# Optimization experiments

Measured on AMD Instinct MI355X. Metric: run time of the kernel, lower is better.

## Reference

```python
import jax, jax.numpy as jnp
import numpy as np

TAU = 2.0      # LIF membrane time constant (spikingjelly default-style, decay_input=True)
VTH = 0.5      # v_threshold from init
S = 4          # time_steps
EPS = 1e-5     # BatchNorm eps
ALPHA = 4.0    # surrogate sigmoid alpha (spikingjelly Sigmoid default)

@jax.custom_vjp
def spike(x):
    # Heaviside forward (spikingjelly: x >= 0 -> 1)
    return (x >= 0.0).astype(x.dtype)

def _spike_fwd(x):
    return spike(x), x

def _spike_bwd(x, g):
    sg = jax.nn.sigmoid(ALPHA * x)
    return (g * ALPHA * sg * (1.0 - sg),)

spike.defvjp(_spike_fwd, _spike_bwd)

def bn(y, gamma, beta, mean, var):
    # inference-mode BatchNorm2d over channel axis 1; y: (B, C, T, V)
    inv = gamma * jax.lax.rsqrt(var + EPS)
    return y * inv[None, :, None, None] + (beta - mean * inv)[None, :, None, None]


def setup_inputs() -> dict:
    key = jax.random.key(0)
    ks = jax.random.split(key, 16)
    B, T, C, V, H, NC = 16, 512, 3, 16, 128, 12
    inp = {
        "x": jax.random.normal(ks[0], (B, T, C, V), dtype=jnp.float32),
        "w1": jax.random.normal(ks[1], (H, C), dtype=jnp.float32) * (1.0 / np.sqrt(C)),
        "b1": jax.random.normal(ks[2], (H,), dtype=jnp.float32) * 0.01,
        "g1": jnp.ones((H,), jnp.float32),
        "be1": jnp.zeros((H,), jnp.float32),
        "m1": jax.random.normal(ks[3], (H,), dtype=jnp.float32) * 0.1,
        "rv1": jax.random.uniform(ks[4], (H,), dtype=jnp.float32) + 0.5,
        "w2": jax.random.normal(ks[5], (H, H), dtype=jnp.float32) * (1.0 / np.sqrt(H)),
        "b2": jax.random.normal(ks[6], (H,), dtype=jnp.float32) * 0.01,
        "g2": jnp.ones((H,), jnp.float32),
        "be2": jnp.zeros((H,), jnp.float32),
        "m2": jax.random.normal(ks[7], (H,), dtype=jnp.float32) * 0.1,
        "rv2": jax.random.uniform(ks[8], (H,), dtype=jnp.float32) + 0.5,
        "wc": jax.random.normal(ks[9], (NC, H), dtype=jnp.float32) * (1.0 / np.sqrt(H)),
        "bc": jax.random.normal(ks[10], (NC,), dtype=jnp.float32) * 0.01,
    }
    return inp


def reference(x, w1, b1, g1, be1, m1, rv1, w2, b2, g2, be2, m2, rv2, wc, bc):
    # x: (B, T, C, V) -> channels-first (B, C, T, V) as in torch permute
    xc = jnp.transpose(x, (0, 2, 1, 3))
    # fc1 1x1 conv + BN; input identical across all S steps, so compute once
    h1 = bn(jnp.einsum('bctv,oc->botv', xc, w1) + b1[None, :, None, None],
            g1, be1, m1, rv1)  # (B, H, T, V)

    def step(carry, _):
        v1s, v2s, acc = carry
        # LIF1: decay_input=True, v_reset=0 hard reset
        v1n = v1s + (h1 - v1s) / TAU
        s1 = spike(v1n - VTH)
        v1n = v1n * (1.0 - s1)
        # fc2 1x1 conv + BN on spikes
        h2 = bn(jnp.einsum('botv,po->bptv', s1, w2) + b2[None, :, None, None],
                g2, be2, m2, rv2)
        # LIF2
        v2n = v2s + (h2 - v2s) / TAU
        s2 = spike(v2n - VTH)
        v2n = v2n * (1.0 - s2)
        return (v1n, v2n, acc + s2), None

    z = jnp.zeros_like(h1)
    (_, _, acc), _ = jax.lax.scan(step, (z, z, z), None, length=S)
    # mean over S, then mean over T and V -> (B, H); dropout is identity in eval
    feat = (acc / S).mean(axis=(2, 3))
    return feat @ wc.T + bc
```

## Files before the change

### kernel.cpp

```cpp
#include <hip/hip_runtime.h>
#include <hip/hip_bf16.h>
#include <stdint.h>
#include <math.h>

#define B_ 16
#define T_ 512
#define V_ 16
#define H_ 128
#define NC_ 12

typedef float v2f __attribute__((ext_vector_type(2)));
typedef __attribute__((ext_vector_type(8))) short s8frag;
typedef __attribute__((ext_vector_type(4))) float f4frag;
typedef unsigned long long u64;


__global__ __launch_bounds__(1024) void zero_feat_kernel(float* __restrict__ feat) {
    int i = blockIdx.x * 1024 + threadIdx.x;
    if (i < B_ * H_) feat[i] = 0.f;
}

__global__ __launch_bounds__(1024, 4) void snn_main(
    const float* __restrict__ x,
    const float* __restrict__ w1, const float* __restrict__ b1,
    const float* __restrict__ g1, const float* __restrict__ be1,
    const float* __restrict__ m1, const float* __restrict__ rv1,
    const float* __restrict__ w2, const float* __restrict__ b2,
    const float* __restrict__ g2, const float* __restrict__ be2,
    const float* __restrict__ m2, const float* __restrict__ rv2,
    float* __restrict__ feat)
{
    __shared__ union {
        unsigned short Bw[2 * H_ * H_];
        uint4 afrag[16 * 4 * 64];
    } u;
    __shared__ u64 mask_lds[64 * 8];
    __shared__ u64 lut[16];
    __shared__ float red[8 * 16];

    const int tid  = threadIdx.x;
    const int lane = tid & 63;
    const int wave = tid >> 6;
    const int b     = blockIdx.x >> 6;
    const int chunk = blockIdx.x & 63;
    const int slice = wave & 7;
    const int kg    = lane >> 4;

    if (tid < 16) {
        u64 v = 0;
        #pragma unroll
        for (int j = 0; j < 4; ++j)
            if ((tid >> j) & 1) v |= (u64)0x3F80u << (16 * j);
        lut[tid] = v;
    }

    for (int i = tid; i < H_ * H_; i += 1024) {
        float w = w2[i];
        __hip_bfloat16 hb = __float2bfloat16(w);
        float hf = __bfloat162float(hb);
        __hip_bfloat16 lb = __float2bfloat16(w - hf);
        u.Bw[i]            = *(unsigned short*)&hb;
        u.Bw[H_ * H_ + i]  = *(unsigned short*)&lb;
    }

    const int p = lane, q = lane + 64;
    v2f w0v = { w1[p*3+0], w1[q*3+0] };
    v2f w1v = { w1[p*3+1], w1[q*3+1] };
    v2f w2v = { w1[p*3+2], w1[q*3+2] };
    v2f b1v = { b1[p], b1[q] };
    float i1a = g1[p] * (float)(1.0 / sqrt((double)(rv1[p] + 1e-5f)));
    float i1b = g1[q] * (float)(1.0 / sqrt((double)(rv1[q] + 1e-5f)));
    v2f i1v = { i1a, i1b };
    v2f d1v = { be1[p] - m1[p] * i1a, be1[q] - m1[q] * i1b };
    const int ch = slice * 16 + (lane & 15);
    float i2c = g2[ch] * (float)(1.0 / sqrt((double)(rv2[ch] + 1e-5f)));
    float d2c = be2[ch] - m2[ch] * i2c;
    float b2c = b2[ch];

    __syncthreads();

    s8frag bhi[4], blo[4];
    #pragma unroll
    for (int c = 0; c < 4; ++c) {
        int idx = ch * H_ + c * 32 + kg * 8;
        bhi[c] = *(const s8frag*)&u.Bw[idx];
        blo[c] = *(const s8frag*)&u.Bw[H_ * H_ + idx];
    }
    __syncthreads();

    float facc = 0.f;
    const int tile_own = wave;
    const int tbase = (wave >> 3) * 8;

    for (int g = 0; g < 2; ++g) {
        #pragma unroll
        for (int i = 0; i < 4; ++i) {
            int sl   = wave + 16 * i;
            int site = chunk * 128 + g * 64 + sl;
            int t = site >> 4, v = site & 15;
            const float* xp = x + ((size_t)(b * T_ + t) * 3) * V_ + v;
            float x0 = xp[0], x1 = xp[V_], x2 = xp[2 * V_];

            v2f h1 = ((x0 * w0v + x1 * w1v + x2 * w2v) + b1v) * i1v + d1v;
            v2f v1t = h1 * 0.5f;
            v2f v2t = v1t + h1 * 0.25f;
            v2f v3t = v2t + (h1 - v2t) * 0.5f;
            v2f v4t = v3t + (h1 - v3t) * 0.5f;

            u64 t1a = __ballot(v1t.x >= 0.5f), t2a = __ballot(v2t.x >= 0.5f);
            u64 t3a = __ballot(v3t.x >= 0.5f), t4a = __ballot(v4t.x >= 0.5f);
            u64 t1b = __ballot(v1t.y >= 0.5f), t2b = __ballot(v2t.y >= 0.5f);
            u64 t3b = __ballot(v3t.y >= 0.5f), t4b = __ballot(v4t.y >= 0.5f);
            u64 s3a = t1a | (t3a & ~t2a), s3b = t1b | (t3b & ~t2b);
            u64 s4a = t2a | (t4a & ~t3a), s4b = t2b | (t4b & ~t3b);

            if (lane < 8) {
                int stp = lane >> 1; bool hf = lane & 1;
                u64 vm;
                if      (stp == 0) vm = hf ? t1b : t1a;
                else if (stp == 1) vm = hf ? t2b : t2a;
                else if (stp == 2) vm = hf ? s3b : s3a;
                else               vm = hf ? s4b : s4a;
                mask_lds[sl * 8 + lane] = vm;
            }
        }
        __syncthreads();

        {
            int r   = lane & 15;
            int sl  = tile_own * 4 + (r >> 2);
            int stp = r & 3;
            const unsigned char* mb = (const unsigned char*)&mask_lds[sl * 8 + stp * 2];
            #pragma unroll
            for (int c = 0; c < 4; ++c) {
                unsigned int bt = mb[c * 4 + kg];
                u64 lo = lut[bt & 15], hi = lut[bt >> 4];
                uint4 fr;
                fr.x = (unsigned)lo; fr.y = (unsigned)(lo >> 32);
                fr.z = (unsigned)hi; fr.w = (unsigned)(hi >> 32);
                u.afrag[(tile_own * 4 + c) * 64 + lane] = fr;
            }
        }
        __syncthreads();

        for (int j = 0; j < 8; ++j) {
            int tl = tbase + j;
            s8frag a0 = *(const s8frag*)&u.afrag[(tl * 4 + 0) * 64 + lane];
            s8frag a1 = *(const s8frag*)&u.afrag[(tl * 4 + 1) * 64 + lane];
            s8frag a2 = *(const s8frag*)&u.afrag[(tl * 4 + 2) * 64 + lane];
            s8frag a3 = *(const s8frag*)&u.afrag[(tl * 4 + 3) * 64 + lane];
            f4frag acc = { 0.f, 0.f, 0.f, 0.f };
            acc = __builtin_amdgcn_mfma_f32_16x16x32_bf16(a0, bhi[0], acc, 0, 0, 0);
            acc = __builtin_amdgcn_mfma_f32_16x16x32_bf16(a1, bhi[1], acc, 0, 0, 0);
            acc = __builtin_amdgcn_mfma_f32_16x16x32_bf16(a2, bhi[2], acc, 0, 0, 0);
            acc = __builtin_amdgcn_mfma_f32_16x16x32_bf16(a3, bhi[3], acc, 0, 0, 0);
            acc = __builtin_amdgcn_mfma_f32_16x16x32_bf16(a0, blo[0], acc, 0, 0, 0);
            acc = __builtin_amdgcn_mfma_f32_16x16x32_bf16(a1, blo[1], acc, 0, 0, 0);
            acc = __builtin_amdgcn_mfma_f32_16x16x32_bf16(a2, blo[2], acc, 0, 0, 0);
            acc = __builtin_amdgcn_mfma_f32_16x16x32_bf16(a3, blo[3], acc, 0, 0, 0);

            float vv = 0.f;
            #pragma unroll
            for (int s = 0; s < 4; ++s) {
                float h2 = (acc[s] + b2c) * i2c + d2c;
                vv = vv + (h2 - vv) * 0.5f;
                bool sp = vv >= 0.5f;
                vv = sp ? 0.f : vv;
                facc += sp ? 1.f : 0.f;
            }
        }
        __syncthreads();
    }

    facc += __shfl_down(facc, 32);
    facc += __shfl_down(facc, 16);
    if (wave < 8) {
        if (lane < 16) red[slice * 16 + lane] = facc;
    }
    __syncthreads();
    if (wave >= 8 && lane < 16) {
        atomicAdd(&feat[b * H_ + ch], red[slice * 16 + lane] + facc);
    }
}

__global__ __launch_bounds__(128) void classifier_kernel(
    const float* __restrict__ feat,
    const float* __restrict__ wc,
    const float* __restrict__ bc,
    float* __restrict__ out) {
    __shared__ float fb[H_];
    int b = blockIdx.x, t = threadIdx.x;
    fb[t] = feat[b * H_ + t] * (1.0f / 32768.0f);
    __syncthreads();
    if (t < NC_) {
        float s = 0.f;
        for (int h = 0; h < H_; ++h) s += fb[h] * wc[t * H_ + h];
        out[b * NC_ + t] = s + bc[t];
    }
}

extern "C" void kernel_launch(void* const* d_in, const int* in_sizes, int n_in,
                              void* d_out, int out_size, void* d_ws, size_t ws_size,
                              hipStream_t stream) {
    const float* x   = (const float*)d_in[0];
    const float* w1  = (const float*)d_in[1];
    const float* b1  = (const float*)d_in[2];
    const float* g1  = (const float*)d_in[3];
    const float* be1 = (const float*)d_in[4];
    const float* m1  = (const float*)d_in[5];
    const float* rv1 = (const float*)d_in[6];
    const float* w2  = (const float*)d_in[7];
    const float* b2  = (const float*)d_in[8];
    const float* g2  = (const float*)d_in[9];
    const float* be2 = (const float*)d_in[10];
    const float* m2  = (const float*)d_in[11];
    const float* rv2 = (const float*)d_in[12];
    const float* wc  = (const float*)d_in[13];
    const float* bc  = (const float*)d_in[14];
    float* feat = (float*)d_ws;
    float* out  = (float*)d_out;

    zero_feat_kernel<<<2, 1024, 0, stream>>>(feat);
    snn_main<<<1024, 1024, 0, stream>>>(x, w1, b1, g1, be1, m1, rv1,
                                        w2, b2, g2, be2, m2, rv2, feat);
    classifier_kernel<<<B_, 128, 0, stream>>>(feat, wc, bc, out);
}
```

Measured before the change: 154.9 us.

## Precompute bf16 split weights once and pipeline spike-mask build with MFMA

Moves the hi/lo bf16 split of w2 into a prep kernel run once per call, so each block loads B fragments straight from global memory instead of rebuilding them in LDS. Blocks shrink to 256 threads, and each wave now owns 32 output channels across all sites. Spike masks are double-buffered in LDS, so the MFMA work for the previous round overlaps fragment construction for the next, with one barrier per round. A bit-arithmetic expand replaces the LUT. The trade is more blocks and more atomics, plus higher register pressure from holding two channel sets of B fragments.

```diff
diff --git a/kernel.cpp b/kernel.cpp
--- a/kernel.cpp
+++ b/kernel.cpp
@@ -14,54 +14,56 @@
 typedef __attribute__((ext_vector_type(4))) float f4frag;
 typedef unsigned long long u64;
 
-
-__global__ __launch_bounds__(1024) void zero_feat_kernel(float* __restrict__ feat) {
-    int i = blockIdx.x * 1024 + threadIdx.x;
+#define WS_W2L_OFF  32768
+#define WS_FEAT_OFF 65536
+
+__global__ __launch_bounds__(256) void prep_kernel(const float* __restrict__ w2,
+                                                   unsigned short* __restrict__ w2h,
+                                                   unsigned short* __restrict__ w2l,
+                                                   float* __restrict__ feat) {
+    int i = blockIdx.x * 256 + threadIdx.x;
+    if (i < H_ * H_) {
+        float w = w2[i];
+        __hip_bfloat16 hb = __float2bfloat16(w);
+        float hf = __bfloat162float(hb);
+        __hip_bfloat16 lb = __float2bfloat16(w - hf);
+        w2h[i] = *(unsigned short*)&hb;
+        w2l[i] = *(unsigned short*)&lb;
+    }
     if (i < B_ * H_) feat[i] = 0.f;
 }
 
-__global__ __launch_bounds__(1024, 4) void snn_main(
+__device__ __forceinline__ uint4 expand8(unsigned bt) {
+    uint4 r;
+    r.x = ((bt      & 1u) * 0x3F80u) | (((bt >> 1) & 1u) * 0x3F800000u);
+    r.y = (((bt >> 2) & 1u) * 0x3F80u) | (((bt >> 3) & 1u) * 0x3F800000u);
+    r.z = (((bt >> 4) & 1u) * 0x3F80u) | (((bt >> 5) & 1u) * 0x3F800000u);
+    r.w = (((bt >> 6) & 1u) * 0x3F80u) | (((bt >> 7) & 1u) * 0x3F800000u);
+    return r;
+}
+
+#define ROUNDS 4
+__global__ __launch_bounds__(256, 3) void snn_main(
     const float* __restrict__ x,
     const float* __restrict__ w1, const float* __restrict__ b1,
     const float* __restrict__ g1, const float* __restrict__ be1,
     const float* __restrict__ m1, const float* __restrict__ rv1,
-    const float* __restrict__ w2, const float* __restrict__ b2,
+    const unsigned short* __restrict__ w2h, const unsigned short* __restrict__ w2l,
+    const float* __restrict__ b2,
     const float* __restrict__ g2, const float* __restrict__ be2,
     const float* __restrict__ m2, const float* __restrict__ rv2,
     float* __restrict__ feat)
 {
-    __shared__ union {
-        unsigned short Bw[2 * H_ * H_];
-        uint4 afrag[16 * 4 * 64];
-    } u;
-    __shared__ u64 mask_lds[64 * 8];
-    __shared__ u64 lut[16];
-    __shared__ float red[8 * 16];
+    __shared__ uint4 afrag[2][4][4][64];
+    __shared__ uint4 msk[4][16];
 
     const int tid  = threadIdx.x;
     const int lane = tid & 63;
-    const int wave = tid >> 6;
-    const int b     = blockIdx.x >> 6;
-    const int chunk = blockIdx.x & 63;
-    const int slice = wave & 7;
-    const int kg    = lane >> 4;
-
-    if (tid < 16) {
-        u64 v = 0;
-        #pragma unroll
-        for (int j = 0; j < 4; ++j)
-            if ((tid >> j) & 1) v |= (u64)0x3F80u << (16 * j);
-        lut[tid] = v;
-    }
-
-    for (int i = tid; i < H_ * H_; i += 1024) {
-        float w = w2[i];
-        __hip_bfloat16 hb = __float2bfloat16(w);
-        float hf = __bfloat162float(hb);
-        __hip_bfloat16 lb = __float2bfloat16(w - hf);
-        u.Bw[i]            = *(unsigned short*)&hb;
-        u.Bw[H_ * H_ + i]  = *(unsigned short*)&lb;
-    }
+    const int wv   = tid >> 6;
+    const int kg   = lane >> 4;
+    const int nl   = lane & 15;
+    const int bb   = blockIdx.x >> 7;
+    const int sbase = (blockIdx.x & 127) * (ROUNDS * 16);
 
     const int p = lane, q = lane + 64;
     v2f w0v = { w1[p*3+0], w1[q*3+0] };
@@ -72,33 +74,71 @@
     float i1b = g1[q] * (float)(1.0 / sqrt((double)(rv1[q] + 1e-5f)));
     v2f i1v = { i1a, i1b };
     v2f d1v = { be1[p] - m1[p] * i1a, be1[q] - m1[q] * i1b };
-    const int ch = slice * 16 + (lane & 15);
-    float i2c = g2[ch] * (float)(1.0 / sqrt((double)(rv2[ch] + 1e-5f)));
-    float d2c = be2[ch] - m2[ch] * i2c;
-    float b2c = b2[ch];
-
-    __syncthreads();
-
-    s8frag bhi[4], blo[4];
+
+    const int ch0 = wv * 32 + nl;
+    const int ch1 = ch0 + 16;
+    float i2c0 = g2[ch0] * (float)(1.0 / sqrt((double)(rv2[ch0] + 1e-5f)));
+    float d2c0 = be2[ch0] - m2[ch0] * i2c0;
+    float b2c0 = b2[ch0];
+    float i2c1 = g2[ch1] * (float)(1.0 / sqrt((double)(rv2[ch1] + 1e-5f)));
+    float d2c1 = be2[ch1] - m2[ch1] * i2c1;
+    float b2c1 = b2[ch1];
+
+    s8frag bh0[4], bl0[4], bh1[4], bl1[4];
     #pragma unroll
     for (int c = 0; c < 4; ++c) {
-        int idx = ch * H_ + c * 32 + kg * 8;
-        bhi[c] = *(const s8frag*)&u.Bw[idx];
-        blo[c] = *(const s8frag*)&u.Bw[H_ * H_ + idx];
-    }
-    __syncthreads();
-
-    float facc = 0.f;
-    const int tile_own = wave;
-    const int tbase = (wave >> 3) * 8;
-
-    for (int g = 0; g < 2; ++g) {
+        int i0 = ch0 * H_ + c * 32 + kg * 8;
+        int i1 = ch1 * H_ + c * 32 + kg * 8;
+        bh0[c] = *(const s8frag*)&w2h[i0];
+        bl0[c] = *(const s8frag*)&w2l[i0];
+        bh1[c] = *(const s8frag*)&w2h[i1];
+        bl1[c] = *(const s8frag*)&w2l[i1];
+    }
+
+    float facc0 = 0.f, facc1 = 0.f;
+
+    #define CONSUME(BUF)                                                        \
+        for (int tt = 0; tt < 4; ++tt) {                                        \
+            s8frag a0 = *(const s8frag*)&afrag[BUF][tt][0][lane];               \
+            s8frag a1 = *(const s8frag*)&afrag[BUF][tt][1][lane];               \
+            s8frag a2 = *(const s8frag*)&afrag[BUF][tt][2][lane];               \
+            s8frag a3 = *(const s8frag*)&afrag[BUF][tt][3][lane];               \
+            f4frag acc0 = {0.f,0.f,0.f,0.f}, acc1 = {0.f,0.f,0.f,0.f};          \
+            acc0 = __builtin_amdgcn_mfma_f32_16x16x32_bf16(a0, bh0[0], acc0, 0,0,0); \
+            acc0 = __builtin_amdgcn_mfma_f32_16x16x32_bf16(a1, bh0[1], acc0, 0,0,0); \
+            acc0 = __builtin_amdgcn_mfma_f32_16x16x32_bf16(a2, bh0[2], acc0, 0,0,0); \
+            acc0 = __builtin_amdgcn_mfma_f32_16x16x32_bf16(a3, bh0[3], acc0, 0,0,0); \
+            acc0 = __builtin_amdgcn_mfma_f32_16x16x32_bf16(a0, bl0[0], acc0, 0,0,0); \
+            acc0 = __builtin_amdgcn_mfma_f32_16x16x32_bf16(a1, bl0[1], acc0, 0,0,0); \
+            acc0 = __builtin_amdgcn_mfma_f32_16x16x32_bf16(a2, bl0[2], acc0, 0,0,0); \
+            acc0 = __builtin_amdgcn_mfma_f32_16x16x32_bf16(a3, bl0[3], acc0, 0,0,0); \
+            acc1 = __builtin_amdgcn_mfma_f32_16x16x32_bf16(a0, bh1[0], acc1, 0,0,0); \
+            acc1 = __builtin_amdgcn_mfma_f32_16x16x32_bf16(a1, bh1[1], acc1, 0,0,0); \
+            acc1 = __builtin_amdgcn_mfma_f32_16x16x32_bf16(a2, bh1[2], acc1, 0,0,0); \
+            acc1 = __builtin_amdgcn_mfma_f32_16x16x32_bf16(a3, bh1[3], acc1, 0,0,0); \
+            acc1 = __builtin_amdgcn_mfma_f32_16x16x32_bf16(a0, bl1[0], acc1, 0,0,0); \
+            acc1 = __builtin_amdgcn_mfma_f32_16x16x32_bf16(a1, bl1[1], acc1, 0,0,0); \
+            acc1 = __builtin_amdgcn_mfma_f32_16x16x32_bf16(a2, bl1[2], acc1, 0,0,0); \
+            acc1 = __builtin_amdgcn_mfma_f32_16x16x32_bf16(a3, bl1[3], acc1, 0,0,0); \
+            float v0 = 0.f, v1 = 0.f;                                           \
+            _Pragma("unroll")                                                   \
+            for (int s = 0; s < 4; ++s) {                                       \
+                float h20 = (acc0[s] + b2c0) * i2c0 + d2c0;                     \
+                float h21 = (acc1[s] + b2c1) * i2c1 + d2c1;                     \
+                v0 = v0 + (h20 - v0) * 0.5f;                                    \
+                v1 = v1 + (h21 - v1) * 0.5f;                                    \
+                bool s0 = v0 >= 0.5f, s1 = v1 >= 0.5f;                          \
+                v0 = s0 ? 0.f : v0;  v1 = s1 ? 0.f : v1;                        \
+                facc0 += s0 ? 1.f : 0.f;  facc1 += s1 ? 1.f : 0.f;              \
+            }                                                                   \
+        }
+
+    for (int r = 0; r < ROUNDS; ++r) {
         #pragma unroll
         for (int i = 0; i < 4; ++i) {
-            int sl   = wave + 16 * i;
-            int site = chunk * 128 + g * 64 + sl;
+            int site = sbase + r * 16 + wv * 4 + i;
             int t = site >> 4, v = site & 15;
-            const float* xp = x + ((size_t)(b * T_ + t) * 3) * V_ + v;
+            const float* xp = x + ((size_t)(bb * T_ + t) * 3) * V_ + v;
             float x0 = xp[0], x1 = xp[V_], x2 = xp[2 * V_];
 
             v2f h1 = ((x0 * w0v + x1 * w1v + x2 * w2v) + b1v) * i1v + d1v;
@@ -114,72 +154,37 @@
             u64 s3a = t1a | (t3a & ~t2a), s3b = t1b | (t3b & ~t2b);
             u64 s4a = t2a | (t4a & ~t3a), s4b = t2b | (t4b & ~t3b);
 
-            if (lane < 8) {
-                int stp = lane >> 1; bool hf = lane & 1;
-                u64 vm;
-                if      (stp == 0) vm = hf ? t1b : t1a;
-                else if (stp == 1) vm = hf ? t2b : t2a;
-                else if (stp == 2) vm = hf ? s3b : s3a;
-                else               vm = hf ? s4b : s4a;
-                mask_lds[sl * 8 + lane] = vm;
+            u64 mx = (lane == 0) ? t1a : (lane == 1) ? t2a : (lane == 2) ? s3a : s4a;
+            u64 my = (lane == 0) ? t1b : (lane == 1) ? t2b : (lane == 2) ? s3b : s4b;
+            if (lane < 4) {
+                uint4 mm;
+                mm.x = (unsigned)mx; mm.y = (unsigned)(mx >> 32);
+                mm.z = (unsigned)my; mm.w = (unsigned)(my >> 32);
+                msk[wv][i * 4 + lane] = mm;
             }
         }
+        {
+            uint4 mm = msk[wv][nl];
+            u64 wx = (u64)mm.x | ((u64)mm.y << 32);
+            u64 wy = (u64)mm.z | ((u64)mm.w << 32);
+            int sh = kg << 3;
+            int buf = r & 1;
+            afrag[buf][wv][0][lane] = expand8((unsigned)(wx >> sh) & 0xFFu);
+            afrag[buf][wv][1][lane] = expand8((unsigned)(wx >> (sh + 32)) & 0xFFu);
+            afrag[buf][wv][2][lane] = expand8((unsigned)(wy >> sh) & 0xFFu);
+            afrag[buf][wv][3][lane] = expand8((unsigned)(wy >> (sh + 32)) & 0xFFu);
+        }
+        if (r > 0) { int pb = (r - 1) & 1; CONSUME(pb); }
         __syncthreads();
-
-        {
-            int r   = lane & 15;
-            int sl  = tile_own * 4 + (r >> 2);
-            int stp = r & 3;
-            const unsigned char* mb = (const unsigned char*)&mask_lds[sl * 8 + stp * 2];
-            #pragma unroll
-            for (int c = 0; c < 4; ++c) {
-                unsigned int bt = mb[c * 4 + kg];
-                u64 lo = lut[bt & 15], hi = lut[bt >> 4];
-                uint4 fr;
-                fr.x = (unsigned)lo; fr.y = (unsigned)(lo >> 32);
-                fr.z = (unsigned)hi; fr.w = (unsigned)(hi >> 32);
-                u.afrag[(tile_own * 4 + c) * 64 + lane] = fr;
-            }
-        }
-        __syncthreads();
-
-        for (int j = 0; j < 8; ++j) {
-            int tl = tbase + j;
-            s8frag a0 = *(const s8frag*)&u.afrag[(tl * 4 + 0) * 64 + lane];
-            s8frag a1 = *(const s8frag*)&u.afrag[(tl * 4 + 1) * 64 + lane];
-            s8frag a2 = *(const s8frag*)&u.afrag[(tl * 4 + 2) * 64 + lane];
-            s8frag a3 = *(const s8frag*)&u.afrag[(tl * 4 + 3) * 64 + lane];
-            f4frag acc = { 0.f, 0.f, 0.f, 0.f };
-            acc = __builtin_amdgcn_mfma_f32_16x16x32_bf16(a0, bhi[0], acc, 0, 0, 0);
-            acc = __builtin_amdgcn_mfma_f32_16x16x32_bf16(a1, bhi[1], acc, 0, 0, 0);
-            acc = __builtin_amdgcn_mfma_f32_16x16x32_bf16(a2, bhi[2], acc, 0, 0, 0);
-            acc = __builtin_amdgcn_mfma_f32_16x16x32_bf16(a3, bhi[3], acc, 0, 0, 0);
-            acc = __builtin_amdgcn_mfma_f32_16x16x32_bf16(a0, blo[0], acc, 0, 0, 0);
-            acc = __builtin_amdgcn_mfma_f32_16x16x32_bf16(a1, blo[1], acc, 0, 0, 0);
-            acc = __builtin_amdgcn_mfma_f32_16x16x32_bf16(a2, blo[2], acc, 0, 0, 0);
-            acc = __builtin_amdgcn_mfma_f32_16x16x32_bf16(a3, blo[3], acc, 0, 0, 0);
-
-            float vv = 0.f;
-            #pragma unroll
-            for (int s = 0; s < 4; ++s) {
-                float h2 = (acc[s] + b2c) * i2c + d2c;
-                vv = vv + (h2 - vv) * 0.5f;
-                bool sp = vv >= 0.5f;
-                vv = sp ? 0.f : vv;
-                facc += sp ? 1.f : 0.f;
-            }
-        }
-        __syncthreads();
-    }
-
-    facc += __shfl_down(facc, 32);
-    facc += __shfl_down(facc, 16);
-    if (wave < 8) {
-        if (lane < 16) red[slice * 16 + lane] = facc;
-    }
-    __syncthreads();
-    if (wave >= 8 && lane < 16) {
-        atomicAdd(&feat[b * H_ + ch], red[slice * 16 + lane] + facc);
+    }
+    { int pb = (ROUNDS - 1) & 1; CONSUME(pb); }
+    #undef CONSUME
+
+    facc0 += __shfl_xor(facc0, 16); facc0 += __shfl_xor(facc0, 32);
+    facc1 += __shfl_xor(facc1, 16); facc1 += __shfl_xor(facc1, 32);
+    if (lane < 16) {
+        atomicAdd(&feat[bb * H_ + ch0], facc0);
+        atomicAdd(&feat[bb * H_ + ch1], facc1);
     }
 }
 
@@ -217,11 +222,14 @@
     const float* rv2 = (const float*)d_in[12];
     const float* wc  = (const float*)d_in[13];
     const float* bc  = (const float*)d_in[14];
-    float* feat = (float*)d_ws;
+
+    unsigned short* w2h = (unsigned short*)d_ws;
+    unsigned short* w2l = (unsigned short*)((char*)d_ws + WS_W2L_OFF);
+    float* feat = (float*)((char*)d_ws + WS_FEAT_OFF);
     float* out  = (float*)d_out;
 
-    zero_feat_kernel<<<2, 1024, 0, stream>>>(feat);
-    snn_main<<<1024, 1024, 0, stream>>>(x, w1, b1, g1, be1, m1, rv1,
-                                        w2, b2, g2, be2, m2, rv2, feat);
+    prep_kernel<<<64, 256, 0, stream>>>(w2, w2h, w2l, feat);
+    snn_main<<<2048, 256, 0, stream>>>(x, w1, b1, g1, be1, m1, rv1,
+                                       w2h, w2l, b2, g2, be2, m2, rv2, feat);
     classifier_kernel<<<B_, 128, 0, stream>>>(feat, wc, bc, out);
 }
```

Result: faster. 145.7 us (-6.0%).
